# Performance work log

Hardware: AMD Instinct MI355X
Metric: run time of the kernel (lower is better)

The kernel has to match this reference:

```python
import jax, jax.numpy as jnp
import numpy as np

B, L, D, P = 2, 1024, 256, 32

def setup_inputs() -> dict:
    key = jax.random.key(0)
    k1, k2, k3, k4, k5 = jax.random.split(key, 5)
    x = jax.random.normal(k1, (B, L, D), dtype=jnp.float32)
    s_in = 1.0 / np.sqrt(D)
    W_phase = jax.random.normal(k2, (D, P), dtype=jnp.float32) * s_in
    b_phase = jax.random.normal(k3, (P,), dtype=jnp.float32) * 0.01
    W_val = jax.random.normal(k4, (D, D), dtype=jnp.float32) * s_in
    b_val = jax.random.normal(k5, (D,), dtype=jnp.float32) * 0.01
    return {"x": x, "W_phase": W_phase, "b_phase": b_phase, "W_val": W_val, "b_val": b_val}

def reference(x, W_phase, b_phase, W_val, b_val):
    # phases: [B, L, P] in (-pi, pi)
    phases = jnp.tanh(x @ W_phase + b_phase) * jnp.float32(np.pi)
    # unit-magnitude complex phasors: [B, L, P]
    phasors = jnp.exp(1j * phases)  # complex64
    # values: [B, L, D]
    values = x @ W_val + b_val
    # bind value vector to each phasor via outer product: [B, L, P, D] complex64
    bound = phasors[..., None] * values[:, :, None, :].astype(jnp.complex64)
    # holographic memory = running sum over sequence position
    memory = jnp.cumsum(bound, axis=1)
    return (memory, phases, phasors)
```

## Files before the change

kernel.cpp:

```cpp
#include <hip/hip_runtime.h>
#include <math.h>

#define B_ 2
#define L_ 1024
#define D_ 256
#define P_ 32
#define NROW (B_*L_)
#define C_ 16
#define CL_ (L_/C_)
#define PIF 3.14159265358979323846f

typedef float nvf4 __attribute__((ext_vector_type(4)));
typedef float nvf2 __attribute__((ext_vector_type(2)));

__global__ __launch_bounds__(256) void k_proj3(
    const float* __restrict__ x, const float* __restrict__ Wp,
    const float* __restrict__ bp, const float* __restrict__ Wv,
    const float* __restrict__ bv, float* __restrict__ values,
    float* __restrict__ phases_out, float* __restrict__ phasor_out,
    float2* __restrict__ phasorT, int phasorMode, int hasPT)
{
    __shared__ float smem[5120];
    const int tid = threadIdx.x;

    if (blockIdx.x < NROW / 4) {
        const int row0 = blockIdx.x * 4;
        float*  xsv = smem;
        float4* red = (float4*)(smem + 1024);

        ((float4*)xsv)[tid] = ((const float4*)(x + (size_t)row0 * D_))[tid];
        __syncthreads();

        const int q  = tid >> 6;
        const int c4 = tid & 63;
        const float4* Wv4 = (const float4*)Wv;
        float4 acc[4];
        #pragma unroll
        for (int r = 0; r < 4; ++r) acc[r] = make_float4(0.f, 0.f, 0.f, 0.f);

        const int k0 = q * 64;
        #pragma unroll 4
        for (int kk = 0; kk < 64; ++kk) {
            const int k = k0 + kk;
            float4 w = Wv4[k * 64 + c4];
            #pragma unroll
            for (int r = 0; r < 4; ++r) {
                float xv = xsv[r * D_ + k];
                acc[r].x += xv * w.x; acc[r].y += xv * w.y;
                acc[r].z += xv * w.z; acc[r].w += xv * w.w;
            }
        }
        #pragma unroll
        for (int r = 0; r < 4; ++r) red[(r * 4 + q) * 64 + c4] = acc[r];
        __syncthreads();

        const int r2 = tid >> 6;
        float4 s0 = red[(r2 * 4 + 0) * 64 + c4];
        float4 s1 = red[(r2 * 4 + 1) * 64 + c4];
        float4 s2 = red[(r2 * 4 + 2) * 64 + c4];
        float4 s3 = red[(r2 * 4 + 3) * 64 + c4];
        const float4 b4 = ((const float4*)bv)[c4];
        float4 out;
        out.x = s0.x + s1.x + s2.x + s3.x + b4.x;
        out.y = s0.y + s1.y + s2.y + s3.y + b4.y;
        out.z = s0.z + s1.z + s2.z + s3.z + b4.z;
        out.w = s0.w + s1.w + s2.w + s3.w + b4.w;
        ((float4*)values)[(size_t)(row0 + r2) * 64 + c4] = out;
    } else {
        const int row0 = (blockIdx.x - NROW / 4) * 8;
        float* xs = smem;
        const float4* xg4 = (const float4*)(x + (size_t)row0 * D_);
        ((float4*)xs)[tid]       = xg4[tid];
        ((float4*)xs)[tid + 256] = xg4[tid + 256];
        __syncthreads();

        const int p  = tid & (P_ - 1);
        const int rr = tid >> 5;
        const float* xr = xs + rr * D_;
        float a = 0.f;
        #pragma unroll 8
        for (int k = 0; k < D_; ++k)
            a += xr[k] * Wp[k * P_ + p];
        float ph = tanhf(a + bp[p]) * PIF;
        const int row = row0 + rr;
        const int idx = row * P_ + p;
        phases_out[idx] = ph;
        float s, c;
        sincosf(ph, &s, &c);
        if (phasorMode == 0) {
            ((float2*)phasor_out)[idx] = make_float2(c, s);
        } else if (phasorMode == 1) {
            phasor_out[idx] = c;
        }
        if (hasPT) {
            const int b = row >> 10, l = row & (L_ - 1);
            phasorT[(b * P_ + p) * L_ + l] = make_float2(c, s);
        }
    }
}

__global__ __launch_bounds__(128) void k_partial(
    const float* __restrict__ values, const float* __restrict__ phases,
    const float2* __restrict__ phasorT, float4* __restrict__ S4, int hasPT)
{
    const int blk = blockIdx.x;
    const int c = blk & (C_ - 1);
    const int p = (blk >> 4) & (P_ - 1);
    const int b = blk >> 9;
    const int tid = threadIdx.x;
    const int l0 = c * CL_;

    __shared__ float2 pc[CL_];
    if (tid < CL_) {
        if (hasPT) {
            pc[tid] = phasorT[(b * P_ + p) * L_ + l0 + tid];
        } else {
            float ph = phases[(b * L_ + l0 + tid) * P_ + p];
            pc[tid] = make_float2(__cosf(ph), __sinf(ph));
        }
    }
    __syncthreads();

    const float2* v2 = (const float2*)(values + (size_t)(b * L_ + l0) * D_);
    float4 acc = make_float4(0.f, 0.f, 0.f, 0.f);
    #pragma unroll 8
    for (int i = 0; i < CL_; ++i) {
        float2 ph = pc[i];
        float2 v  = v2[i * (D_/2) + tid];
        acc.x += ph.x * v.x;
        acc.y += ph.y * v.x;
        acc.z += ph.x * v.y;
        acc.w += ph.y * v.y;
    }
    S4[((b * P_ + p) * C_ + c) * (D_/2) + tid] = acc;
}

__global__ __launch_bounds__(128) void k_scan(
    const float* __restrict__ values, const float* __restrict__ phases,
    const float2* __restrict__ phasorT, const float4* __restrict__ S4,
    float* __restrict__ mem, int mode, int hasPT)
{
    const int blk = blockIdx.x;
    const int c = blk & (C_ - 1);
    const int p = (blk >> 4) & (P_ - 1);
    const int b = blk >> 9;
    const int tid = threadIdx.x;
    const int l0 = c * CL_;

    __shared__ float2 pc[CL_];
    if (tid < CL_) {
        if (hasPT) {
            pc[tid] = phasorT[(b * P_ + p) * L_ + l0 + tid];
        } else {
            float ph = phases[(b * L_ + l0 + tid) * P_ + p];
            pc[tid] = make_float2(__cosf(ph), __sinf(ph));
        }
    }

    float4 carry = make_float4(0.f, 0.f, 0.f, 0.f);
    const float4* Sbase = S4 + (size_t)(b * P_ + p) * C_ * (D_/2) + tid;
    for (int cc = 0; cc < c; ++cc) {
        float4 s = Sbase[cc * (D_/2)];
        carry.x += s.x; carry.y += s.y; carry.z += s.z; carry.w += s.w;
    }
    __syncthreads();

    const float2* v2 = (const float2*)(values + (size_t)(b * L_ + l0) * D_);
    #pragma unroll 8
    for (int i = 0; i < CL_; ++i) {
        float2 ph = pc[i];
        float2 v  = v2[i * (D_/2) + tid];
        carry.x += ph.x * v.x;
        carry.y += ph.y * v.x;
        carry.z += ph.x * v.y;
        carry.w += ph.y * v.y;
        const size_t rowIdx = (size_t)(b * L_ + l0 + i) * P_ + p;
        if (mode == 0) {
            nvf4 cv = { carry.x, carry.y, carry.z, carry.w };
            __builtin_nontemporal_store(cv, (nvf4*)mem + rowIdx * (D_/2) + tid);
        } else {
            nvf2 cv = { carry.x, carry.z };
            __builtin_nontemporal_store(cv, (nvf2*)mem + rowIdx * (D_/2) + tid);
        }
    }
}

__global__ __launch_bounds__(128) void k_scan_rc(
    const float* __restrict__ values, const float* __restrict__ phases,
    float* __restrict__ mem, int mode)
{
    const int blk = blockIdx.x;
    const int c = blk & (C_ - 1);
    const int p = (blk >> 4) & (P_ - 1);
    const int b = blk >> 9;
    const int tid = threadIdx.x;
    const int l0 = c * CL_;

    const float2* vb = (const float2*)(values + (size_t)b * L_ * D_);
    float4 carry = make_float4(0.f, 0.f, 0.f, 0.f);
    for (int l = 0; l < l0; ++l) {
        float ph = phases[(b * L_ + l) * P_ + p];
        float s = __sinf(ph), cs = __cosf(ph);
        float2 v = vb[l * (D_/2) + tid];
        carry.x += cs * v.x; carry.y += s * v.x;
        carry.z += cs * v.y; carry.w += s * v.y;
    }
    for (int i = 0; i < CL_; ++i) {
        const int l = l0 + i;
        float ph = phases[(b * L_ + l) * P_ + p];
        float s = __sinf(ph), cs = __cosf(ph);
        float2 v = vb[l * (D_/2) + tid];
        carry.x += cs * v.x; carry.y += s * v.x;
        carry.z += cs * v.y; carry.w += s * v.y;
        const size_t rowIdx = (size_t)(b * L_ + l) * P_ + p;
        if (mode == 0) ((float4*)mem)[rowIdx * (D_/2) + tid] = carry;
        else ((float2*)mem)[rowIdx * (D_/2) + tid] = make_float2(carry.x, carry.z);
    }
}

extern "C" void kernel_launch(void* const* d_in, const int* in_sizes, int n_in,
                              void* d_out, int out_size, void* d_ws, size_t ws_size,
                              hipStream_t stream) {
    const float* x  = (const float*)d_in[0];
    const float* Wp = (const float*)d_in[1];
    const float* bp = (const float*)d_in[2];
    const float* Wv = (const float*)d_in[3];
    const float* bv = (const float*)d_in[4];
    float* out = (float*)d_out;

    const size_t nMemF = (size_t)2 * B_ * L_ * P_ * D_;
    const size_t nMemR = (size_t)B_ * L_ * P_ * D_;
    const size_t nPh   = (size_t)B_ * L_ * P_;

    int mode; size_t memFloats;
    if ((size_t)out_size >= nMemF + 3 * nPh) { mode = 0; memFloats = nMemF; }
    else                                     { mode = 1; memFloats = nMemR; }
    const bool memFits      = (size_t)out_size >= memFloats;
    const bool phasesInOut  = (size_t)out_size >= memFloats + nPh;
    const bool phasorsInOut =
        (size_t)out_size >= memFloats + nPh + (mode == 0 ? 2 * nPh : nPh);

    const size_t valB = (size_t)B_ * L_ * D_ * sizeof(float);
    const size_t phB  = nPh * sizeof(float);
    const size_t s4B  = (size_t)B_ * P_ * C_ * (D_/2) * sizeof(float4);
    const size_t ptB  = (size_t)B_ * P_ * L_ * sizeof(float2);
    float*  values   = (float*)d_ws;
    float*  phasesWs = (float*)((char*)d_ws + valB);
    float4* S4       = (float4*)((char*)d_ws + valB + phB);
    float2* phasorT  = (float2*)((char*)d_ws + valB + phB + s4B);

    float* phasesPtr = phasesInOut ? (out + memFloats)
                     : (ws_size >= valB + phB ? phasesWs : nullptr);
    if (phasesPtr == nullptr) return;

    float* phasorPtr = phasorsInOut ? (out + memFloats + nPh) : nullptr;
    const int phasorMode = phasorsInOut ? mode : 2;

    const bool pathA = ws_size >= valB + phB + s4B;
    const int  hasPT = (pathA && ws_size >= valB + phB + s4B + ptB) ? 1 : 0;

    k_proj3<<<NROW / 4 + NROW / 8, 256, 0, stream>>>(
        x, Wp, bp, Wv, bv, values, phasesPtr, phasorPtr, phasorT,
        phasorMode, hasPT);
    if (!memFits) return;

    if (pathA) {
        k_partial<<<B_ * P_ * C_, 128, 0, stream>>>(values, phasesPtr, phasorT,
                                                    S4, hasPT);
        k_scan<<<B_ * P_ * C_, 128, 0, stream>>>(values, phasesPtr, phasorT,
                                                 S4, out, mode, hasPT);
    } else {
        k_scan_rc<<<B_ * P_ * C_, 128, 0, stream>>>(values, phasesPtr, out, mode);
    }
}
```

Measured before the change: 110.6 us.

## Specialize real-only mode, shrink projection tiles, use fast tanh and sincos

Adds a real-only (mode 1) path to the partial and scan kernels. That path stores and uses only cosine phasors and accumulates two components instead of four, which removes unused imaginary arithmetic and halves the phasorT traffic. The value projection now uses 2-row blocks with k unrolled by 4 and float4 x reads, giving more blocks. The phase projection uses 4 independent accumulators and a fast exp-based tanh with __sincosf. The fast intrinsics add precision risk, and the 2-row tiles reread W_val more often.

```diff
diff --git a/kernel.cpp b/kernel.cpp
--- a/kernel.cpp
+++ b/kernel.cpp
@@ -18,56 +18,65 @@
     const float* __restrict__ bp, const float* __restrict__ Wv,
     const float* __restrict__ bv, float* __restrict__ values,
     float* __restrict__ phases_out, float* __restrict__ phasor_out,
-    float2* __restrict__ phasorT, int phasorMode, int hasPT)
+    float* __restrict__ phasorT, int phasorMode, int mode, int hasPT)
 {
-    __shared__ float smem[5120];
+    __shared__ float smem[2560];
     const int tid = threadIdx.x;
 
-    if (blockIdx.x < NROW / 4) {
-        const int row0 = blockIdx.x * 4;
+    if (blockIdx.x < NROW / 2) {
+        const int row0 = blockIdx.x * 2;
         float*  xsv = smem;
-        float4* red = (float4*)(smem + 1024);
-
-        ((float4*)xsv)[tid] = ((const float4*)(x + (size_t)row0 * D_))[tid];
+        float4* red = (float4*)(smem + 512);
+
+        if (tid < 128)
+            ((float4*)xsv)[tid] = ((const float4*)(x + (size_t)row0 * D_))[tid];
         __syncthreads();
 
         const int q  = tid >> 6;
         const int c4 = tid & 63;
         const float4* Wv4 = (const float4*)Wv;
-        float4 acc[4];
-        #pragma unroll
-        for (int r = 0; r < 4; ++r) acc[r] = make_float4(0.f, 0.f, 0.f, 0.f);
+        float4 acc0 = make_float4(0.f, 0.f, 0.f, 0.f);
+        float4 acc1 = make_float4(0.f, 0.f, 0.f, 0.f);
 
         const int k0 = q * 64;
-        #pragma unroll 4
-        for (int kk = 0; kk < 64; ++kk) {
+        for (int kk = 0; kk < 64; kk += 4) {
             const int k = k0 + kk;
-            float4 w = Wv4[k * 64 + c4];
-            #pragma unroll
-            for (int r = 0; r < 4; ++r) {
-                float xv = xsv[r * D_ + k];
-                acc[r].x += xv * w.x; acc[r].y += xv * w.y;
-                acc[r].z += xv * w.z; acc[r].w += xv * w.w;
-            }
-        }
-        #pragma unroll
-        for (int r = 0; r < 4; ++r) red[(r * 4 + q) * 64 + c4] = acc[r];
-        __syncthreads();
-
-        const int r2 = tid >> 6;
-        float4 s0 = red[(r2 * 4 + 0) * 64 + c4];
-        float4 s1 = red[(r2 * 4 + 1) * 64 + c4];
-        float4 s2 = red[(r2 * 4 + 2) * 64 + c4];
-        float4 s3 = red[(r2 * 4 + 3) * 64 + c4];
-        const float4 b4 = ((const float4*)bv)[c4];
-        float4 out;
-        out.x = s0.x + s1.x + s2.x + s3.x + b4.x;
-        out.y = s0.y + s1.y + s2.y + s3.y + b4.y;
-        out.z = s0.z + s1.z + s2.z + s3.z + b4.z;
-        out.w = s0.w + s1.w + s2.w + s3.w + b4.w;
-        ((float4*)values)[(size_t)(row0 + r2) * 64 + c4] = out;
-    } else {
-        const int row0 = (blockIdx.x - NROW / 4) * 8;
+            float4 w0 = Wv4[(k + 0) * 64 + c4];
+            float4 w1 = Wv4[(k + 1) * 64 + c4];
+            float4 w2 = Wv4[(k + 2) * 64 + c4];
+            float4 w3 = Wv4[(k + 3) * 64 + c4];
+            float4 xa = *(const float4*)(xsv + 0 * D_ + k);
+            float4 xb = *(const float4*)(xsv + 1 * D_ + k);
+            acc0.x += xa.x*w0.x + xa.y*w1.x + xa.z*w2.x + xa.w*w3.x;
+            acc0.y += xa.x*w0.y + xa.y*w1.y + xa.z*w2.y + xa.w*w3.y;
+            acc0.z += xa.x*w0.z + xa.y*w1.z + xa.z*w2.z + xa.w*w3.z;
+            acc0.w += xa.x*w0.w + xa.y*w1.w + xa.z*w2.w + xa.w*w3.w;
+            acc1.x += xb.x*w0.x + xb.y*w1.x + xb.z*w2.x + xb.w*w3.x;
+            acc1.y += xb.x*w0.y + xb.y*w1.y + xb.z*w2.y + xb.w*w3.y;
+            acc1.z += xb.x*w0.z + xb.y*w1.z + xb.z*w2.z + xb.w*w3.z;
+            acc1.w += xb.x*w0.w + xb.y*w1.w + xb.z*w2.w + xb.w*w3.w;
+        }
+        red[(0 * 4 + q) * 64 + c4] = acc0;
+        red[(1 * 4 + q) * 64 + c4] = acc1;
+        __syncthreads();
+
+        if (tid < 128) {
+            const int r2 = tid >> 6;
+            const int cb = tid & 63;
+            float4 s0 = red[(r2 * 4 + 0) * 64 + cb];
+            float4 s1 = red[(r2 * 4 + 1) * 64 + cb];
+            float4 s2 = red[(r2 * 4 + 2) * 64 + cb];
+            float4 s3 = red[(r2 * 4 + 3) * 64 + cb];
+            const float4 b4 = ((const float4*)bv)[cb];
+            float4 o;
+            o.x = s0.x + s1.x + s2.x + s3.x + b4.x;
+            o.y = s0.y + s1.y + s2.y + s3.y + b4.y;
+            o.z = s0.z + s1.z + s2.z + s3.z + b4.z;
+            o.w = s0.w + s1.w + s2.w + s3.w + b4.w;
+            ((float4*)values)[(size_t)(row0 + r2) * 64 + cb] = o;
+        }
+    } else {
+        const int row0 = (blockIdx.x - NROW / 2) * 8;
         float* xs = smem;
         const float4* xg4 = (const float4*)(x + (size_t)row0 * D_);
         ((float4*)xs)[tid]       = xg4[tid];
@@ -77,16 +86,29 @@
         const int p  = tid & (P_ - 1);
         const int rr = tid >> 5;
         const float* xr = xs + rr * D_;
-        float a = 0.f;
-        #pragma unroll 8
-        for (int k = 0; k < D_; ++k)
-            a += xr[k] * Wp[k * P_ + p];
-        float ph = tanhf(a + bp[p]) * PIF;
+        float a0 = 0.f, a1 = 0.f, a2 = 0.f, a3 = 0.f;
+        for (int k = 0; k < D_; k += 8) {
+            float w0 = Wp[(k + 0) * P_ + p];
+            float w1 = Wp[(k + 1) * P_ + p];
+            float w2 = Wp[(k + 2) * P_ + p];
+            float w3 = Wp[(k + 3) * P_ + p];
+            float w4 = Wp[(k + 4) * P_ + p];
+            float w5 = Wp[(k + 5) * P_ + p];
+            float w6 = Wp[(k + 6) * P_ + p];
+            float w7 = Wp[(k + 7) * P_ + p];
+            float4 xA = *(const float4*)(xr + k);
+            float4 xB = *(const float4*)(xr + k + 4);
+            a0 += xA.x * w0; a1 += xA.y * w1; a2 += xA.z * w2; a3 += xA.w * w3;
+            a0 += xB.x * w4; a1 += xB.y * w5; a2 += xB.z * w6; a3 += xB.w * w7;
+        }
+        float a = (a0 + a1) + (a2 + a3) + bp[p];
+        float e  = __expf(2.0f * a);
+        float ph = (1.0f - __fdividef(2.0f, e + 1.0f)) * PIF;
         const int row = row0 + rr;
         const int idx = row * P_ + p;
         phases_out[idx] = ph;
         float s, c;
-        sincosf(ph, &s, &c);
+        __sincosf(ph, &s, &c);
         if (phasorMode == 0) {
             ((float2*)phasor_out)[idx] = make_float2(c, s);
         } else if (phasorMode == 1) {
@@ -94,14 +116,17 @@
         }
         if (hasPT) {
             const int b = row >> 10, l = row & (L_ - 1);
-            phasorT[(b * P_ + p) * L_ + l] = make_float2(c, s);
+            const size_t ti = (size_t)(b * P_ + p) * L_ + l;
+            if (mode == 1) phasorT[ti] = c;
+            else ((float2*)phasorT)[ti] = make_float2(c, s);
         }
     }
 }
 
 __global__ __launch_bounds__(128) void k_partial(
     const float* __restrict__ values, const float* __restrict__ phases,
-    const float2* __restrict__ phasorT, float4* __restrict__ S4, int hasPT)
+    const float* __restrict__ phasorT, float* __restrict__ S,
+    int mode, int hasPT)
 {
     const int blk = blockIdx.x;
     const int c = blk & (C_ - 1);
@@ -109,35 +134,56 @@
     const int b = blk >> 9;
     const int tid = threadIdx.x;
     const int l0 = c * CL_;
-
-    __shared__ float2 pc[CL_];
-    if (tid < CL_) {
-        if (hasPT) {
-            pc[tid] = phasorT[(b * P_ + p) * L_ + l0 + tid];
+    const int bp = b * P_ + p;
+
+    __shared__ float pcs[2 * CL_];
+    if (hasPT) {
+        if (mode == 1) {
+            if (tid < CL_ / 4)
+                ((float4*)pcs)[tid] =
+                    ((const float4*)(phasorT + (size_t)bp * L_ + l0))[tid];
         } else {
+            if (tid < CL_ / 2)
+                ((float4*)pcs)[tid] = ((const float4*)
+                    ((const float2*)phasorT + (size_t)bp * L_ + l0))[tid];
+        }
+    } else {
+        if (tid < CL_) {
             float ph = phases[(b * L_ + l0 + tid) * P_ + p];
-            pc[tid] = make_float2(__cosf(ph), __sinf(ph));
+            if (mode == 1) pcs[tid] = __cosf(ph);
+            else ((float2*)pcs)[tid] = make_float2(__cosf(ph), __sinf(ph));
         }
     }
     __syncthreads();
 
-    const float2* v2 = (const float2*)(values + (size_t)(b * L_ + l0) * D_);
-    float4 acc = make_float4(0.f, 0.f, 0.f, 0.f);
-    #pragma unroll 8
-    for (int i = 0; i < CL_; ++i) {
-        float2 ph = pc[i];
-        float2 v  = v2[i * (D_/2) + tid];
-        acc.x += ph.x * v.x;
-        acc.y += ph.y * v.x;
-        acc.z += ph.x * v.y;
-        acc.w += ph.y * v.y;
-    }
-    S4[((b * P_ + p) * C_ + c) * (D_/2) + tid] = acc;
+    const float2* vp = (const float2*)(values + (size_t)(b * L_ + l0) * D_) + tid;
+
+    if (mode == 1) {
+        float sx = 0.f, sy = 0.f;
+        #pragma unroll
+        for (int i = 0; i < CL_; ++i) {
+            float pc = pcs[i];
+            float2 v = vp[(size_t)i * (D_/2)];
+            sx += pc * v.x;
+            sy += pc * v.y;
+        }
+        ((float2*)S)[((size_t)bp * C_ + c) * (D_/2) + tid] = make_float2(sx, sy);
+    } else {
+        float4 a = make_float4(0.f, 0.f, 0.f, 0.f);
+        #pragma unroll
+        for (int i = 0; i < CL_; ++i) {
+            float2 q = ((float2*)pcs)[i];
+            float2 v = vp[(size_t)i * (D_/2)];
+            a.x += q.x * v.x; a.y += q.y * v.x;
+            a.z += q.x * v.y; a.w += q.y * v.y;
+        }
+        ((float4*)S)[((size_t)bp * C_ + c) * (D_/2) + tid] = a;
+    }
 }
 
 __global__ __launch_bounds__(128) void k_scan(
     const float* __restrict__ values, const float* __restrict__ phases,
-    const float2* __restrict__ phasorT, const float4* __restrict__ S4,
+    const float* __restrict__ phasorT, const float* __restrict__ S,
     float* __restrict__ mem, int mode, int hasPT)
 {
     const int blk = blockIdx.x;
@@ -146,41 +192,66 @@
     const int b = blk >> 9;
     const int tid = threadIdx.x;
     const int l0 = c * CL_;
-
-    __shared__ float2 pc[CL_];
-    if (tid < CL_) {
-        if (hasPT) {
-            pc[tid] = phasorT[(b * P_ + p) * L_ + l0 + tid];
+    const int bp = b * P_ + p;
+
+    __shared__ float pcs[2 * CL_];
+    if (hasPT) {
+        if (mode == 1) {
+            if (tid < CL_ / 4)
+                ((float4*)pcs)[tid] =
+                    ((const float4*)(phasorT + (size_t)bp * L_ + l0))[tid];
         } else {
+            if (tid < CL_ / 2)
+                ((float4*)pcs)[tid] = ((const float4*)
+                    ((const float2*)phasorT + (size_t)bp * L_ + l0))[tid];
+        }
+    } else {
+        if (tid < CL_) {
             float ph = phases[(b * L_ + l0 + tid) * P_ + p];
-            pc[tid] = make_float2(__cosf(ph), __sinf(ph));
-        }
-    }
-
-    float4 carry = make_float4(0.f, 0.f, 0.f, 0.f);
-    const float4* Sbase = S4 + (size_t)(b * P_ + p) * C_ * (D_/2) + tid;
-    for (int cc = 0; cc < c; ++cc) {
-        float4 s = Sbase[cc * (D_/2)];
-        carry.x += s.x; carry.y += s.y; carry.z += s.z; carry.w += s.w;
-    }
-    __syncthreads();
-
-    const float2* v2 = (const float2*)(values + (size_t)(b * L_ + l0) * D_);
-    #pragma unroll 8
-    for (int i = 0; i < CL_; ++i) {
-        float2 ph = pc[i];
-        float2 v  = v2[i * (D_/2) + tid];
-        carry.x += ph.x * v.x;
-        carry.y += ph.y * v.x;
-        carry.z += ph.x * v.y;
-        carry.w += ph.y * v.y;
-        const size_t rowIdx = (size_t)(b * L_ + l0 + i) * P_ + p;
-        if (mode == 0) {
-            nvf4 cv = { carry.x, carry.y, carry.z, carry.w };
-            __builtin_nontemporal_store(cv, (nvf4*)mem + rowIdx * (D_/2) + tid);
-        } else {
-            nvf2 cv = { carry.x, carry.z };
-            __builtin_nontemporal_store(cv, (nvf2*)mem + rowIdx * (D_/2) + tid);
+            if (mode == 1) pcs[tid] = __cosf(ph);
+            else ((float2*)pcs)[tid] = make_float2(__cosf(ph), __sinf(ph));
+        }
+    }
+
+    const float2* vp = (const float2*)(values + (size_t)(b * L_ + l0) * D_) + tid;
+
+    if (mode == 1) {
+        float cx = 0.f, cz = 0.f;
+        const float2* Sb = (const float2*)S + (size_t)bp * C_ * (D_/2) + tid;
+        for (int cc = 0; cc < c; ++cc) {
+            float2 s = Sb[(size_t)cc * (D_/2)];
+            cx += s.x; cz += s.y;
+        }
+        __syncthreads();
+        nvf2* dst = (nvf2*)mem + ((size_t)(b * L_ + l0) * P_ + p) * (D_/2) + tid;
+        const size_t st = (size_t)P_ * (D_/2);
+        #pragma unroll
+        for (int i = 0; i < CL_; ++i) {
+            float pc = pcs[i];
+            float2 v = vp[(size_t)i * (D_/2)];
+            cx += pc * v.x;
+            cz += pc * v.y;
+            nvf2 o = { cx, cz };
+            __builtin_nontemporal_store(o, dst + (size_t)i * st);
+        }
+    } else {
+        float4 carry = make_float4(0.f, 0.f, 0.f, 0.f);
+        const float4* Sb = (const float4*)S + (size_t)bp * C_ * (D_/2) + tid;
+        for (int cc = 0; cc < c; ++cc) {
+            float4 s = Sb[(size_t)cc * (D_/2)];
+            carry.x += s.x; carry.y += s.y; carry.z += s.z; carry.w += s.w;
+        }
+        __syncthreads();
+        nvf4* dst = (nvf4*)mem + ((size_t)(b * L_ + l0) * P_ + p) * (D_/2) + tid;
+        const size_t st = (size_t)P_ * (D_/2);
+        #pragma unroll
+        for (int i = 0; i < CL_; ++i) {
+            float2 q = ((float2*)pcs)[i];
+            float2 v = vp[(size_t)i * (D_/2)];
+            carry.x += q.x * v.x; carry.y += q.y * v.x;
+            carry.z += q.x * v.y; carry.w += q.y * v.y;
+            nvf4 o = { carry.x, carry.y, carry.z, carry.w };
+            __builtin_nontemporal_store(o, dst + (size_t)i * st);
         }
     }
 }
@@ -242,12 +313,12 @@
 
     const size_t valB = (size_t)B_ * L_ * D_ * sizeof(float);
     const size_t phB  = nPh * sizeof(float);
-    const size_t s4B  = (size_t)B_ * P_ * C_ * (D_/2) * sizeof(float4);
-    const size_t ptB  = (size_t)B_ * P_ * L_ * sizeof(float2);
-    float*  values   = (float*)d_ws;
-    float*  phasesWs = (float*)((char*)d_ws + valB);
-    float4* S4       = (float4*)((char*)d_ws + valB + phB);
-    float2* phasorT  = (float2*)((char*)d_ws + valB + phB + s4B);
+    const size_t sB   = (size_t)B_ * P_ * C_ * (D_/2) * sizeof(float4);
+    const size_t ptB  = nPh * (mode == 0 ? sizeof(float2) : sizeof(float));
+    float* values   = (float*)d_ws;
+    float* phasesWs = (float*)((char*)d_ws + valB);
+    float* S        = (float*)((char*)d_ws + valB + phB);
+    float* phasorT  = (float*)((char*)d_ws + valB + phB + sB);
 
     float* phasesPtr = phasesInOut ? (out + memFloats)
                      : (ws_size >= valB + phB ? phasesWs : nullptr);
@@ -256,19 +327,19 @@
     float* phasorPtr = phasorsInOut ? (out + memFloats + nPh) : nullptr;
     const int phasorMode = phasorsInOut ? mode : 2;
 
-    const bool pathA = ws_size >= valB + phB + s4B;
-    const int  hasPT = (pathA && ws_size >= valB + phB + s4B + ptB) ? 1 : 0;
-
-    k_proj3<<<NROW / 4 + NROW / 8, 256, 0, stream>>>(
+    const bool pathA = ws_size >= valB + phB + sB;
+    const int  hasPT = (pathA && ws_size >= valB + phB + sB + ptB) ? 1 : 0;
+
+    k_proj3<<<NROW / 2 + NROW / 8, 256, 0, stream>>>(
         x, Wp, bp, Wv, bv, values, phasesPtr, phasorPtr, phasorT,
-        phasorMode, hasPT);
+        phasorMode, mode, hasPT);
     if (!memFits) return;
 
     if (pathA) {
         k_partial<<<B_ * P_ * C_, 128, 0, stream>>>(values, phasesPtr, phasorT,
-                                                    S4, hasPT);
+                                                    S, mode, hasPT);
         k_scan<<<B_ * P_ * C_, 128, 0, stream>>>(values, phasesPtr, phasorT,
-                                                 S4, out, mode, hasPT);
+                                                 S, out, mode, hasPT);
     } else {
         k_scan_rc<<<B_ * P_ * C_, 128, 0, stream>>>(values, phasesPtr, out, mode);
     }
```

After: 107.9 us. 1.02x faster.
